# Kernel optimization log

Hardware: AMD Instinct MI355X
Metric: run time of the kernel (lower is better)

The kernel has to match this reference:

```python
import jax, jax.numpy as jnp
import numpy as np
import math

B, T, C = 2, 2048, 1024
H = 16
D = C // H

def setup_inputs() -> dict:
    key = jax.random.key(0)
    k1, k2, k3, k4, k5 = jax.random.split(key, 5)
    scale = 0.02
    return {
        "x": jax.random.normal(k1, (B, T, C), dtype=jnp.float32),
        "w_attn": jax.random.normal(k2, (3 * C, C), dtype=jnp.float32) * scale,
        "b_attn": jax.random.normal(k3, (3 * C,), dtype=jnp.float32) * scale,
        "w_proj": jax.random.normal(k4, (C, C), dtype=jnp.float32) * scale,
        "b_proj": jax.random.normal(k5, (C,), dtype=jnp.float32) * scale,
    }

def reference(x, w_attn, b_attn, w_proj, b_proj):
    b, t, c = x.shape
    # c_attn: torch Linear -> x @ W.T + b, output [b, t, 3c]
    qkv = jnp.einsum('btc,fc->btf', x, w_attn) + b_attn
    # einops 'b t (a h d) -> a b h t d' with a=3, h=H
    qkv = qkv.reshape(b, t, 3, H, D).transpose(2, 0, 3, 1, 4)
    q, k, v = qkv[0], qkv[1], qkv[2]  # each [b, h, t, d]
    att = jnp.einsum('bhtd,bhsd->bhts', q, k) * (1.0 / math.sqrt(D))
    # causal mask: positions s > t are masked
    mask = jnp.tril(jnp.ones((t, t), dtype=bool))
    att = jnp.where(mask[None, None, :, :], att, jnp.float32(-jnp.inf))
    att = jax.nn.softmax(att, axis=-1)
    y = jnp.einsum('bhts,bhsd->bhtd', att, v)  # [b, h, t, d]
    y = y.transpose(0, 2, 1, 3).reshape(b, t, c)
    return jnp.einsum('btc,fc->btf', y, w_proj) + b_proj
```

## Files before the change

kernel.cpp:

```cpp
#include <hip/hip_runtime.h>
#include <stdint.h>

typedef unsigned short u16;
typedef __attribute__((ext_vector_type(8))) __bf16 bvec8;
typedef __attribute__((ext_vector_type(4))) float f32x4;

__device__ __forceinline__ u16 f32_to_bf16(float f) {
    uint32_t u = __float_as_uint(f);
    u += 0x7fffu + ((u >> 16) & 1u);
    return (u16)(u >> 16);
}

__device__ __forceinline__ void gl2lds16(const u16* g, u16* l) {
    void* gnc = const_cast<void*>((const void*)g);
    __builtin_amdgcn_global_load_lds(
        (__attribute__((address_space(1))) uint32_t*)gnc,
        (__attribute__((address_space(3))) uint32_t*)((void*)l),
        16, 0, 0);
}

__global__ __launch_bounds__(256) void cvt3(
    const float* __restrict__ a, int na4, const float* __restrict__ b, int nb4,
    const float* __restrict__ c, int nc4,
    u16* __restrict__ oa, u16* __restrict__ ob, u16* __restrict__ oc)
{
    int i = blockIdx.x * 256 + threadIdx.x;
    const float* src; u16* dst; int off;
    if (i < na4)             { src = a; dst = oa; off = i; }
    else if (i < na4 + nb4)  { src = b; dst = ob; off = i - na4; }
    else if (i < na4 + nb4 + nc4) { src = c; dst = oc; off = i - na4 - nb4; }
    else return;
    float4 v = ((const float4*)src)[off];
    ushort4 o;
    o.x = f32_to_bf16(v.x); o.y = f32_to_bf16(v.y);
    o.z = f32_to_bf16(v.z); o.w = f32_to_bf16(v.w);
    ((ushort4*)dst)[off] = o;
}

template <int BNt, bool OUT_BF16>
__global__ __launch_bounds__(256) void gemm_bt_bias(
    const u16* __restrict__ A, const u16* __restrict__ B,
    const float* __restrict__ bias, void* __restrict__ Cv,
    int M, int N, int K)
{
    constexpr int NT = BNt / 32;
    __shared__ __attribute__((aligned(16))) u16 As[128 * 32];
    __shared__ __attribute__((aligned(16))) u16 Bs[BNt * 32];

    const int tid = threadIdx.x, wave = tid >> 6, lane = tid & 63;
    const int col = lane & 15, quad = lane >> 4;
    const int m0 = blockIdx.y * 128, n0 = blockIdx.x * BNt;
    const int wm = (wave >> 1) * 64, wn = (wave & 1) * (BNt / 2);
    const int srow = lane >> 2, schunk = lane & 3;
    const u16* Ag = A + (size_t)(m0 + wave * 32) * K;

    f32x4 acc[4][NT];
#pragma unroll
    for (int i = 0; i < 4; i++)
#pragma unroll
        for (int j = 0; j < NT; j++) acc[i][j] = f32x4{0.f, 0.f, 0.f, 0.f};

    for (int k0 = 0; k0 < K; k0 += 32) {
        __syncthreads();
        gl2lds16(Ag + (size_t)(srow)      * K + k0 + schunk * 8, &As[(wave * 2 + 0) * 512]);
        gl2lds16(Ag + (size_t)(16 + srow) * K + k0 + schunk * 8, &As[(wave * 2 + 1) * 512]);
        if constexpr (BNt == 128) {
            const u16* Bg = B + (size_t)(n0 + wave * 32) * K;
            gl2lds16(Bg + (size_t)(srow)      * K + k0 + schunk * 8, &Bs[(wave * 2 + 0) * 512]);
            gl2lds16(Bg + (size_t)(16 + srow) * K + k0 + schunk * 8, &Bs[(wave * 2 + 1) * 512]);
        } else {
            const u16* Bg = B + (size_t)(n0 + wave * 16) * K;
            gl2lds16(Bg + (size_t)(srow)      * K + k0 + schunk * 8, &Bs[wave * 512]);
        }
        __syncthreads();

        bvec8 af[4], bfv[NT];
#pragma unroll
        for (int mt = 0; mt < 4; mt++)  af[mt]  = *(const bvec8*)&As[(wm + mt * 16 + col) * 32 + quad * 8];
#pragma unroll
        for (int nt = 0; nt < NT; nt++) bfv[nt] = *(const bvec8*)&Bs[(wn + nt * 16 + col) * 32 + quad * 8];
#pragma unroll
        for (int mt = 0; mt < 4; mt++)
#pragma unroll
            for (int nt = 0; nt < NT; nt++)
                acc[mt][nt] = __builtin_amdgcn_mfma_f32_16x16x32_bf16(af[mt], bfv[nt], acc[mt][nt], 0, 0, 0);
    }

#pragma unroll
    for (int mt = 0; mt < 4; mt++) {
#pragma unroll
        for (int r = 0; r < 4; r++) {
            const int m = m0 + wm + mt * 16 + quad * 4 + r;
#pragma unroll
            for (int nt = 0; nt < NT; nt++) {
                const int n = n0 + wn + nt * 16 + col;
                float v = acc[mt][nt][r] + bias[n];
                if (OUT_BF16) ((u16*)Cv)[(size_t)m * N + n] = f32_to_bf16(v);
                else          ((float*)Cv)[(size_t)m * N + n] = v;
            }
        }
    }
}

__global__ __launch_bounds__(256) void transpose_v(const u16* __restrict__ qkv,
                                                   u16* __restrict__ vT)
{
    __shared__ u16 Ts[64 * 74];
    const int tid = threadIdx.x;
    const int t0 = blockIdx.x * 64, h = blockIdx.y, b = blockIdx.z;
    const u16* src = qkv + (size_t)b * 2048 * 3072 + 2048 + h * 64;
#pragma unroll
    for (int k2 = 0; k2 < 2; k2++) {
        int c = k2 * 256 + tid, tl = c >> 3, ch = c & 7;
        *(uint4*)&Ts[tl * 74 + ch * 8] = *(const uint4*)(src + (size_t)(t0 + tl) * 3072 + ch * 8);
    }
    __syncthreads();
    u16* dst = vT + (size_t)((b * 16 + h) * 64) * 2048;
#pragma unroll
    for (int k2 = 0; k2 < 2; k2++) {
        int c = k2 * 256 + tid, d = c >> 3, tch = c & 7;
        u16 tmp[8];
#pragma unroll
        for (int j2 = 0; j2 < 8; j2++) tmp[j2] = Ts[(tch * 8 + j2) * 74 + d];
        *(uint4*)&dst[(size_t)d * 2048 + t0 + tch * 8] = *(const uint4*)tmp;
    }
}

__global__ __launch_bounds__(256) void attn_kernel(const u16* __restrict__ qkv,
                                                   const u16* __restrict__ vT,
                                                   u16* __restrict__ Y)
{
    __shared__ __attribute__((aligned(16))) u16 Qs[64 * 64];
    __shared__ __attribute__((aligned(16))) u16 Ks[64 * 64];
    __shared__ __attribute__((aligned(16))) u16 Vs[64 * 64];
    __shared__ __attribute__((aligned(16))) u16 Ps[4 * 16 * 72];

    const int tid = threadIdx.x, wave = tid >> 6, lane = tid & 63;
    const int col = lane & 15, quad = lane >> 4;

    const int s_idx = blockIdx.x;
    const int h = blockIdx.y, b = blockIdx.z;

    const u16* qb = qkv + (size_t)b * 2048 * 3072;
    const u16* vb = vT + (size_t)((b * 16 + h) * 64) * 2048;

    const int c0 = wave * 64 + lane, c1 = 256 + c0;
    const int r0 = c0 >> 3, p0 = c0 & 7, r1 = c1 >> 3, p1 = c1 & 7;
    const int sw0 = (p0 ^ (r0 & 7)) * 8, sw1 = (p1 ^ (r1 & 7)) * 8;

    const int tloc = wave * 16 + quad * 4;

#pragma unroll
    for (int phase = 0; phase < 2; ++phase) {
        const int qt = phase ? (31 - s_idx) : s_idx;
        const int q0 = qt * 64;

        __syncthreads();
        gl2lds16(qb + (size_t)(q0 + r0) * 3072 + h * 64 + sw0, &Qs[wave * 512]);
        gl2lds16(qb + (size_t)(q0 + r1) * 3072 + h * 64 + sw1, &Qs[2048 + wave * 512]);
        __syncthreads();

        const int qrow = wave * 16 + col;
        bvec8 qf0 = *(const bvec8*)&Qs[qrow * 64 + ((quad       ^ (qrow & 7)) * 8)];
        bvec8 qf1 = *(const bvec8*)&Qs[qrow * 64 + (((4 + quad) ^ (qrow & 7)) * 8)];

        float l_acc[4] = {0.f, 0.f, 0.f, 0.f};
        f32x4 o[4];
#pragma unroll
        for (int d = 0; d < 4; d++) o[d] = f32x4{0.f, 0.f, 0.f, 0.f};

        for (int kt = 0; kt <= qt; ++kt) {
            const int s0 = kt * 64;
            __syncthreads();
            gl2lds16(qb + (size_t)(s0 + r0) * 3072 + 1024 + h * 64 + sw0, &Ks[wave * 512]);
            gl2lds16(qb + (size_t)(s0 + r1) * 3072 + 1024 + h * 64 + sw1, &Ks[2048 + wave * 512]);
            gl2lds16(vb + (size_t)r0 * 2048 + s0 + sw0, &Vs[wave * 512]);
            gl2lds16(vb + (size_t)r1 * 2048 + s0 + sw1, &Vs[2048 + wave * 512]);
            __syncthreads();

            f32x4 sv[4];
#pragma unroll
            for (int nt = 0; nt < 4; nt++) {
                const int krow = nt * 16 + col;
                bvec8 kf0 = *(const bvec8*)&Ks[krow * 64 + ((quad       ^ (krow & 7)) * 8)];
                bvec8 kf1 = *(const bvec8*)&Ks[krow * 64 + (((4 + quad) ^ (krow & 7)) * 8)];
                sv[nt] = f32x4{0.f, 0.f, 0.f, 0.f};
                sv[nt] = __builtin_amdgcn_mfma_f32_16x16x32_bf16(qf0, kf0, sv[nt], 0, 0, 0);
                sv[nt] = __builtin_amdgcn_mfma_f32_16x16x32_bf16(qf1, kf1, sv[nt], 0, 0, 0);
            }

            const bool diag = (kt == qt);
            u16* pw = &Ps[wave * 16 * 72];
#pragma unroll
            for (int nt = 0; nt < 4; nt++) {
#pragma unroll
                for (int r = 0; r < 4; r++) {
                    float p = __expf(sv[nt][r] * 0.125f);
                    if (diag && (nt * 16 + col) > (tloc + r)) p = 0.f;
                    l_acc[r] += p;
                    pw[(quad * 4 + r) * 72 + nt * 16 + col] = f32_to_bf16(p);
                }
            }

#pragma unroll
            for (int ks = 0; ks < 2; ks++) {
                bvec8 pf = *(const bvec8*)&Ps[wave * 16 * 72 + col * 72 + ks * 32 + quad * 8];
#pragma unroll
                for (int d = 0; d < 4; d++) {
                    const int vrow = d * 16 + col;
                    bvec8 vf = *(const bvec8*)&Vs[vrow * 64 + (((ks * 4 + quad) ^ (vrow & 7)) * 8)];
                    o[d] = __builtin_amdgcn_mfma_f32_16x16x32_bf16(pf, vf, o[d], 0, 0, 0);
                }
            }
        }

#pragma unroll
        for (int r = 0; r < 4; r++) {
            float s = l_acc[r];
            s += __shfl_xor(s, 1); s += __shfl_xor(s, 2);
            s += __shfl_xor(s, 4); s += __shfl_xor(s, 8);
            const float inv = 1.0f / s;
            const int t = q0 + wave * 16 + quad * 4 + r;
#pragma unroll
            for (int d = 0; d < 4; d++)
                Y[(size_t)(b * 2048 + t) * 1024 + h * 64 + d * 16 + col] =
                    f32_to_bf16(o[d][r] * inv);
        }
    }
}

extern "C" void kernel_launch(void* const* d_in, const int* in_sizes, int n_in,
                              void* d_out, int out_size, void* d_ws, size_t ws_size,
                              hipStream_t stream) {
    const float* x      = (const float*)d_in[0];
    const float* w_attn = (const float*)d_in[1];
    const float* b_attn = (const float*)d_in[2];
    const float* w_proj = (const float*)d_in[3];
    const float* b_proj = (const float*)d_in[4];
    float* out = (float*)d_out;

    u16* xb  = (u16*)d_ws;
    u16* wab = xb  + (size_t)4096 * 1024;
    u16* wpb = wab + (size_t)3072 * 1024;
    u16* qkv = wpb + (size_t)1024 * 1024;
    u16* y   = qkv + (size_t)4096 * 3072;
    u16* vT  = xb;

    const int na4 = 4096 * 1024 / 4, nb4 = 3072 * 1024 / 4, nc4 = 1024 * 1024 / 4;
    cvt3<<<(na4 + nb4 + nc4 + 255) / 256, 256, 0, stream>>>(
        x, na4, w_attn, nb4, w_proj, nc4, xb, wab, wpb);

    dim3 g1(3072 / 128, 4096 / 128);
    gemm_bt_bias<128, true><<<g1, 256, 0, stream>>>(xb, wab, b_attn, qkv, 4096, 3072, 1024);

    dim3 gt(32, 16, 2);
    transpose_v<<<gt, 256, 0, stream>>>(qkv, vT);

    dim3 g2(16, 16, 2);
    attn_kernel<<<g2, 256, 0, stream>>>(qkv, vT, y);

    dim3 g3(1024 / 64, 4096 / 128);
    gemm_bt_bias<64, false><<<g3, 256, 0, stream>>>(y, wpb, b_proj, out, 4096, 1024, 1024);
}
```

Before: 198.2 us.

## Double-buffer K/V tiles in attention and reorder grid by batch-head

Attention now keeps two LDS buffers for K and V and issues the global-to-LDS loads for the next key tile before computing on the current one. Explicit vmcnt waits and raw s_barrier replace the paired __syncthreads, so load latency can overlap the MFMA and softmax work. The grid is also remapped so blockIdx.x walks batch*head and blockIdx.y walks query tiles, which changes how blocks are dispatched and which data shares L2. LDS use grows by 16KB per block, and the hand-written waitcnt/barrier sequence depends on the exact number of outstanding loads, which is fragile if the compiler emits other vector memory ops in between.

```diff
diff --git a/kernel.cpp b/kernel.cpp
--- a/kernel.cpp
+++ b/kernel.cpp
@@ -131,18 +131,19 @@
                                                    u16* __restrict__ Y)
 {
     __shared__ __attribute__((aligned(16))) u16 Qs[64 * 64];
-    __shared__ __attribute__((aligned(16))) u16 Ks[64 * 64];
-    __shared__ __attribute__((aligned(16))) u16 Vs[64 * 64];
+    __shared__ __attribute__((aligned(16))) u16 Ks[2][64 * 64];
+    __shared__ __attribute__((aligned(16))) u16 Vs[2][64 * 64];
     __shared__ __attribute__((aligned(16))) u16 Ps[4 * 16 * 72];
 
     const int tid = threadIdx.x, wave = tid >> 6, lane = tid & 63;
     const int col = lane & 15, quad = lane >> 4;
 
-    const int s_idx = blockIdx.x;
-    const int h = blockIdx.y, b = blockIdx.z;
+    const int g = blockIdx.x;
+    const int b = g >> 4, h = g & 15;
+    const int s_idx = blockIdx.y;
 
     const u16* qb = qkv + (size_t)b * 2048 * 3072;
-    const u16* vb = vT + (size_t)((b * 16 + h) * 64) * 2048;
+    const u16* vb = vT + (size_t)g * 64 * 2048;
 
     const int c0 = wave * 64 + lane, c1 = 256 + c0;
     const int r0 = c0 >> 3, p0 = c0 & 7, r1 = c1 >> 3, p1 = c1 & 7;
@@ -169,21 +170,34 @@
 #pragma unroll
         for (int d = 0; d < 4; d++) o[d] = f32x4{0.f, 0.f, 0.f, 0.f};
 
+        {
+            gl2lds16(qb + (size_t)(r0) * 3072 + 1024 + h * 64 + sw0, &Ks[0][wave * 512]);
+            gl2lds16(qb + (size_t)(r1) * 3072 + 1024 + h * 64 + sw1, &Ks[0][2048 + wave * 512]);
+            gl2lds16(vb + (size_t)r0 * 2048 + sw0, &Vs[0][wave * 512]);
+            gl2lds16(vb + (size_t)r1 * 2048 + sw1, &Vs[0][2048 + wave * 512]);
+        }
+
         for (int kt = 0; kt <= qt; ++kt) {
-            const int s0 = kt * 64;
-            __syncthreads();
-            gl2lds16(qb + (size_t)(s0 + r0) * 3072 + 1024 + h * 64 + sw0, &Ks[wave * 512]);
-            gl2lds16(qb + (size_t)(s0 + r1) * 3072 + 1024 + h * 64 + sw1, &Ks[2048 + wave * 512]);
-            gl2lds16(vb + (size_t)r0 * 2048 + s0 + sw0, &Vs[wave * 512]);
-            gl2lds16(vb + (size_t)r1 * 2048 + s0 + sw1, &Vs[2048 + wave * 512]);
-            __syncthreads();
+            const int cur = kt & 1;
+            if (kt < qt) {
+                const int s0n = (kt + 1) * 64;
+                const int nb2 = cur ^ 1;
+                gl2lds16(qb + (size_t)(s0n + r0) * 3072 + 1024 + h * 64 + sw0, &Ks[nb2][wave * 512]);
+                gl2lds16(qb + (size_t)(s0n + r1) * 3072 + 1024 + h * 64 + sw1, &Ks[nb2][2048 + wave * 512]);
+                gl2lds16(vb + (size_t)r0 * 2048 + s0n + sw0, &Vs[nb2][wave * 512]);
+                gl2lds16(vb + (size_t)r1 * 2048 + s0n + sw1, &Vs[nb2][2048 + wave * 512]);
+                asm volatile("s_waitcnt vmcnt(4)" ::: "memory");
+            } else {
+                asm volatile("s_waitcnt vmcnt(0)" ::: "memory");
+            }
+            asm volatile("s_barrier" ::: "memory");
 
             f32x4 sv[4];
 #pragma unroll
             for (int nt = 0; nt < 4; nt++) {
                 const int krow = nt * 16 + col;
-                bvec8 kf0 = *(const bvec8*)&Ks[krow * 64 + ((quad       ^ (krow & 7)) * 8)];
-                bvec8 kf1 = *(const bvec8*)&Ks[krow * 64 + (((4 + quad) ^ (krow & 7)) * 8)];
+                bvec8 kf0 = *(const bvec8*)&Ks[cur][krow * 64 + ((quad       ^ (krow & 7)) * 8)];
+                bvec8 kf1 = *(const bvec8*)&Ks[cur][krow * 64 + (((4 + quad) ^ (krow & 7)) * 8)];
                 sv[nt] = f32x4{0.f, 0.f, 0.f, 0.f};
                 sv[nt] = __builtin_amdgcn_mfma_f32_16x16x32_bf16(qf0, kf0, sv[nt], 0, 0, 0);
                 sv[nt] = __builtin_amdgcn_mfma_f32_16x16x32_bf16(qf1, kf1, sv[nt], 0, 0, 0);
@@ -208,10 +222,11 @@
 #pragma unroll
                 for (int d = 0; d < 4; d++) {
                     const int vrow = d * 16 + col;
-                    bvec8 vf = *(const bvec8*)&Vs[vrow * 64 + (((ks * 4 + quad) ^ (vrow & 7)) * 8)];
+                    bvec8 vf = *(const bvec8*)&Vs[cur][vrow * 64 + (((ks * 4 + quad) ^ (vrow & 7)) * 8)];
                     o[d] = __builtin_amdgcn_mfma_f32_16x16x32_bf16(pf, vf, o[d], 0, 0, 0);
                 }
             }
+            asm volatile("s_barrier" ::: "memory");
         }
 
 #pragma unroll
@@ -256,7 +271,7 @@
     dim3 gt(32, 16, 2);
     transpose_v<<<gt, 256, 0, stream>>>(qkv, vT);
 
-    dim3 g2(16, 16, 2);
+    dim3 g2(32, 16, 1);
     attn_kernel<<<g2, 256, 0, stream>>>(qkv, vT, y);
 
     dim3 g3(1024 / 64, 4096 / 128);
```

Measured after the change: 193.1 us. 2.6% less time.
